# Kernel tuning notes

Hardware: AMD Instinct MI355X
Metric: run time of the kernel (lower is better)

Reference implementation:

```python
import jax, jax.numpy as jnp
import numpy as np

N_NODES = 100000
N_EDGES = 1600000
N_RELS = 19
DIMS = [1, 128, 128, 64]  # in_degree feature -> dims


def setup_inputs() -> dict:
    key = jax.random.key(0)
    ks = jax.random.split(key, 12)
    src = jax.random.randint(ks[0], (N_EDGES,), 0, N_NODES, dtype=jnp.int64)
    dst = jax.random.randint(ks[1], (N_EDGES,), 0, N_NODES, dtype=jnp.int64)
    etypes = jax.random.randint(ks[2], (N_EDGES,), 0, N_RELS, dtype=jnp.int64)
    inp = {"src": src, "dst": dst, "etypes": etypes}
    for i, (din, dout) in enumerate(zip(DIMS[:-1], DIMS[1:])):
        s = 1.0 / np.sqrt(max(din, 1))
        inp[f"W{i}"] = jax.random.normal(ks[3 + 3 * i], (N_RELS, din, dout), jnp.float32) * s
        inp[f"Wloop{i}"] = jax.random.normal(ks[4 + 3 * i], (din, dout), jnp.float32) * s
        inp[f"b{i}"] = jnp.zeros((dout,), jnp.float32)
    inp["num_nodes"] = N_NODES
    return inp


def _rel_graph_conv(h, src, dst, etypes, W, Wloop, b, num_nodes, activation):
    # per-relation transform of every node: [N, R, dout]
    transformed = jnp.einsum('nd,rdo->nro', h, W)
    # gather message per edge by (src node, edge relation): [E, dout]
    msg = transformed[src, etypes]
    # scatter-sum to destination nodes
    agg = jax.ops.segment_sum(msg, dst, num_segments=num_nodes)
    out = agg + h @ Wloop + b
    if activation is not None:
        out = activation(out)
    return out


def reference(src, dst, etypes, W0, Wloop0, b0, W1, Wloop1, b1, W2, Wloop2, b2, num_nodes):
    # h = g.in_degrees().view(-1, 1).float()
    deg = jax.ops.segment_sum(jnp.ones_like(dst, dtype=jnp.float32), dst,
                              num_segments=num_nodes)
    h = deg[:, None]
    h = _rel_graph_conv(h, src, dst, etypes, W0, Wloop0, b0, num_nodes, jax.nn.relu)
    h = _rel_graph_conv(h, src, dst, etypes, W1, Wloop1, b1, num_nodes, jax.nn.relu)
    h = _rel_graph_conv(h, src, dst, etypes, W2, Wloop2, b2, num_nodes, None)
    return h
```

## Files before the change

kernel.cpp:

```cpp
#include <hip/hip_runtime.h>
#include <hip/hip_bf16.h>
#include <stdint.h>

#define N_NODES 100000
#define N_EDGES 1600000
#define N_RELS  19
#define NQ      4
#define QN      25000
#define QTILES  196
#define NBQ     98
#define NSB     (NQ * NBQ)
#define N_BUCK  (NQ * N_RELS)
#define NBIN    391
#define NGR     8
#define NBK8    (N_BUCK * NGR)
#define NBIN8   (NBIN * NGR)
#define NHC     (N_BUCK + NBIN)
#define NHC2    (2 * NHC)
#define MSGQ    460000
#define NCKQ    3700
#define NCK_TOT 14000
#define EPB     2048
#define S1B     782

typedef __attribute__((ext_vector_type(8))) short bf16x8;
typedef __attribute__((ext_vector_type(4))) float f32x4;
typedef __attribute__((ext_vector_type(4))) int   int4v;

__device__ __forceinline__ unsigned short f2bf(float x) {
  union { float f; unsigned u; } v; v.f = x;
  unsigned r = v.u + 0x7FFF + ((v.u >> 16) & 1);
  return (unsigned short)(r >> 16);
}
__device__ __forceinline__ float bf2f(unsigned short b) {
  union { unsigned u; float f; } v; v.u = ((unsigned)b) << 16; return v.f;
}

__global__ void k_prep_w(const float* W1, const float* W2,
                         const float* Wl1, const float* Wl2,
                         unsigned short* Wt1, unsigned short* Wt2,
                         unsigned short* Wtl1, unsigned short* Wtl2) {
  int i = blockIdx.x * 256 + threadIdx.x;
  const int s1 = N_RELS * 128 * 128;
  const int s2 = N_RELS * 64 * 128;
  const int s3 = 128 * 128;
  const int s4 = 64 * 128;
  if (i < s1) {
    int r = i / (128 * 128); int rem = i % (128 * 128);
    int n = rem / 128, k = rem % 128;
    Wt1[i] = f2bf(W1[((size_t)r * 128 + k) * 128 + n]);
  } else if (i < s1 + s2) {
    int j = i - s1;
    int r = j / (64 * 128); int rem = j % (64 * 128);
    int n = rem / 128, k = rem % 128;
    Wt2[j] = f2bf(W2[((size_t)r * 128 + k) * 64 + n]);
  } else if (i < s1 + s2 + s3) {
    int j = i - s1 - s2; int n = j / 128, k = j % 128;
    Wtl1[j] = f2bf(Wl1[k * 128 + n]);
  } else if (i < s1 + s2 + s3 + s4) {
    int j = i - s1 - s2 - s3; int n = j / 128, k = j % 128;
    Wtl2[j] = f2bf(Wl2[k * 64 + n]);
  }
}

__global__ void k_hist(const int* __restrict__ dst, const int* __restrict__ et,
                       int* __restrict__ bcount8, int* __restrict__ bincount8,
                       int* __restrict__ histAll) {
  __shared__ int hK[N_BUCK], hB[NBIN];
  __shared__ int sb[256];
  int t = threadIdx.x, g = blockIdx.x & (NGR - 1);
  for (int i = t; i < N_BUCK; i += 256) hK[i] = 0;
  for (int i = t; i < NBIN; i += 256) hB[i] = 0;
  __syncthreads();
  int e0 = blockIdx.x * EPB;
  for (int r = 0; r < EPB / 256; r++) {
    int e = e0 + r * 256 + t;
    if (e < N_EDGES) {
      int d = dst[e];
      atomicAdd(&hK[(d / QN) * N_RELS + et[e]], 1);
      atomicAdd(&hB[d >> 8], 1);
    }
  }
  __syncthreads();
  int* hout = histAll + (size_t)blockIdx.x * NHC2;
  for (int i = t; i < N_BUCK; i += 256) {
    hout[i] = hK[i];
    if (hK[i]) atomicAdd(&bcount8[i * NGR + g], hK[i]);
  }
  for (int i = t; i < NBIN; i += 256) {
    hout[N_BUCK + i] = hB[i];
    if (hB[i]) atomicAdd(&bincount8[i * NGR + g], hB[i]);
  }
  {
    int v0 = (2 * t < N_BUCK) ? hK[2 * t] : 0;
    int v1 = (2 * t + 1 < N_BUCK) ? hK[2 * t + 1] : 0;
    sb[t] = v0 + v1;
    __syncthreads();
    for (int s = 1; s < 256; s <<= 1) {
      int x = (t >= s) ? sb[t - s] : 0;
      __syncthreads();
      sb[t] += x;
      __syncthreads();
    }
    int base = sb[t] - v0 - v1;
    if (2 * t < N_BUCK) hout[NHC + 2 * t] = base;
    if (2 * t + 1 < N_BUCK) hout[NHC + 2 * t + 1] = base + v0;
    __syncthreads();
  }
  {
    int v0 = (2 * t < NBIN) ? hB[2 * t] : 0;
    int v1 = (2 * t + 1 < NBIN) ? hB[2 * t + 1] : 0;
    sb[t] = v0 + v1;
    __syncthreads();
    for (int s = 1; s < 256; s <<= 1) {
      int x = (t >= s) ? sb[t - s] : 0;
      __syncthreads();
      sb[t] += x;
      __syncthreads();
    }
    int base = sb[t] - v0 - v1;
    if (2 * t < NBIN) hout[NHC + N_BUCK + 2 * t] = base;
    if (2 * t + 1 < NBIN) hout[NHC + N_BUCK + 2 * t + 1] = base + v0;
  }
}

__global__ void k_scan0(const int* __restrict__ bcount8, const int* __restrict__ bincount8,
                        int* boff, int* bcur8, int* cbase, int* qcs, int* selfb,
                        int* binoff8, int* bincur8) {
  __shared__ int shK[NBK8];
  __shared__ int sb76[N_BUCK];
  __shared__ int sbs[N_BUCK];
  __shared__ int sh[512];
  int t = threadIdx.x;
  for (int i = t; i < NBK8; i += 512) shK[i] = bcount8[i];
  __syncthreads();
  if (t < N_BUCK) {
    int s = 0;
    for (int gg = 0; gg < NGR; gg++) s += shK[t * NGR + gg];
    sb76[t] = s;
  }
  __syncthreads();
  if (t == 0) {
    int a = 0, cb = 0;
    for (int q = 0; q < NQ; q++) {
      qcs[q] = cb;
      for (int r = 0; r < N_RELS; r++) {
        int b = q * N_RELS + r;
        boff[b] = a; sbs[b] = a; cbase[b] = cb;
        a += sb76[b]; cb += (sb76[b] + 127) >> 7;
      }
      selfb[q] = cb; cb += QTILES;
    }
    qcs[NQ] = cb;
    boff[N_BUCK] = a;
  }
  __syncthreads();
  for (int i = t; i < NBK8; i += 512) {
    int b = i >> 3, gg = i & (NGR - 1);
    int base = sbs[b];
    for (int k = 0; k < gg; k++) base += shK[b * NGR + k];
    bcur8[i] = base;
  }
  int vals[7];
  int i0 = t * 7;
  int loc = 0;
  for (int k = 0; k < 7; k++) {
    int i = i0 + k;
    int v = (i < NBIN8) ? bincount8[i] : 0;
    vals[k] = v; loc += v;
  }
  sh[t] = loc;
  __syncthreads();
  for (int s = 1; s < 512; s <<= 1) {
    int x = (t >= s) ? sh[t - s] : 0;
    __syncthreads();
    sh[t] += x;
    __syncthreads();
  }
  int run = sh[t] - loc;
  for (int k = 0; k < 7; k++) {
    int i = i0 + k;
    if (i < NBIN8) { binoff8[i] = run; bincur8[i] = run; run += vals[k]; }
  }
  if (t == 511) binoff8[NBIN8] = sh[511];
}

__launch_bounds__(256)
__global__ void k_scat1a(const int* __restrict__ src, const int* __restrict__ dst,
                         const int* __restrict__ et,
                         const int* __restrict__ histAll,
                         int* __restrict__ bcur8,
                         int* __restrict__ srcS, int* __restrict__ posE) {
  __shared__ int sortK[EPB];
  __shared__ int lK[N_BUCK], gKr[N_BUCK];
  int t = threadIdx.x, blk = blockIdx.x, g = blk & (NGR - 1);
  const int* hin = histAll + (size_t)blk * NHC2;
  for (int i = t; i < N_BUCK; i += 256) {
    int h = hin[i], l = hin[NHC + i];
    lK[i] = l;
    gKr[i] = h ? (atomicAdd(&bcur8[i * NGR + g], h) - l) : 0;
  }
  __syncthreads();
  int e0 = blk * EPB;
  int nval = min(EPB, N_EDGES - e0);
  for (int r = 0; r < EPB / 256; r++) {
    int e = e0 + r * 256 + t;
    if (e < N_EDGES) {
      int d = dst[e], rl = et[e], sv = src[e];
      int bk = (d / QN) * N_RELS + rl;
      int lrk = atomicAdd(&lK[bk], 1);
      sortK[lrk] = sv | (bk << 17);
      posE[e] = gKr[bk] + lrk;
    }
  }
  __syncthreads();
  for (int r = 0; r < EPB / 256; r++) {
    int s = r * 256 + t;
    if (s < nval) {
      int v = sortK[s];
      srcS[gKr[v >> 17] + s] = v & 0x1FFFF;
    }
  }
}

__launch_bounds__(256)
__global__ void k_scat1b(const int* __restrict__ src, const int* __restrict__ dst,
                         const int* __restrict__ et,
                         const int* __restrict__ posE,
                         const int* __restrict__ histAll,
                         int* __restrict__ bincur8,
                         int* __restrict__ stgA, int* __restrict__ stgB) {
  __shared__ int sortA[EPB], sortBv[EPB];
  __shared__ int lB[NBIN], gBr[NBIN];
  int t = threadIdx.x, blk = blockIdx.x, g = blk & (NGR - 1);
  const int* hin = histAll + (size_t)blk * NHC2;
  for (int i = t; i < NBIN; i += 256) {
    int h = hin[N_BUCK + i], l = hin[NHC + N_BUCK + i];
    lB[i] = l;
    gBr[i] = h ? (atomicAdd(&bincur8[i * NGR + g], h) - l) : 0;
  }
  __syncthreads();
  int e0 = blk * EPB;
  int nval = min(EPB, N_EDGES - e0);
  for (int r = 0; r < EPB / 256; r++) {
    int e = e0 + r * 256 + t;
    if (e < N_EDGES) {
      int d = dst[e], rl = et[e], sv = src[e];
      int gpos = posE[e];
      int bn = d >> 8;
      int lrb = atomicAdd(&lB[bn], 1);
      sortA[lrb] = gpos | (rl << 21) | ((bn & 63) << 26);
      sortBv[lrb] = sv | ((d & 255) << 17) | ((bn >> 6) << 25);
    }
  }
  __syncthreads();
  for (int r = 0; r < EPB / 256; r++) {
    int s = r * 256 + t;
    if (s < nval) {
      int a = sortA[s], b = sortBv[s];
      int bn = ((a >> 26) & 63) | (((b >> 25) & 7) << 6);
      int adr = gBr[bn] + s;
      stgA[adr] = a & 0x03FFFFFF;
      stgB[adr] = b & 0x01FFFFFF;
    }
  }
}

__global__ void k_cnt(const int* __restrict__ stgB, const int* __restrict__ binoff8,
                      int* __restrict__ ncount) {
  __shared__ int c[256];
  int b = blockIdx.x, t = threadIdx.x;
  c[t] = 0;
  __syncthreads();
  int lo = binoff8[b * NGR], hi = binoff8[b * NGR + NGR];
  for (int s = lo + t; s < hi; s += 256)
    atomicAdd(&c[(stgB[s] >> 17) & 255], 1);
  __syncthreads();
  int n = b * 256 + t;
  if (n < N_NODES) ncount[n] = c[t];
}

__global__ void k_scanA(const int* __restrict__ ncount, int* __restrict__ bsum) {
  __shared__ int sh[256];
  int b = blockIdx.x, t = threadIdx.x;
  int q = b / NBQ, bb = b % NBQ;
  int i = bb * 256 + t;
  int val = (i < QN) ? (ncount[q * QN + i] + 1) : 0;
  sh[t] = val;
  __syncthreads();
  for (int s = 128; s > 0; s >>= 1) {
    if (t < s) sh[t] += sh[t + s];
    __syncthreads();
  }
  if (t == 0) bsum[b] = sh[0];
}

__global__ void k_scanB(const int* bsum, int* bbase, int* nodeoff) {
  __shared__ int sh[NSB];
  int t = threadIdx.x;
  if (t < NSB) sh[t] = bsum[t];
  __syncthreads();
  if (t < NQ) {
    int a = 0;
    for (int i = 0; i < NBQ; i++) {
      int v = sh[t * NBQ + i]; sh[t * NBQ + i] = a; a += v;
    }
    nodeoff[(t + 1) * QN + t] = a;
  }
  __syncthreads();
  if (t < NSB) bbase[t] = sh[t];
}

__global__ void k_scanC(const int* __restrict__ ncount,
                        const int* __restrict__ bbase,
                        const int* __restrict__ boff,
                        int* __restrict__ nodeoff, int* __restrict__ gfwd) {
  __shared__ int sh[256];
  int b = blockIdx.x, t = threadIdx.x;
  int q = b / NBQ, bb = b % NBQ;
  int i = bb * 256 + t;
  int val = (i < QN) ? (ncount[q * QN + i] + 1) : 0;
  sh[t] = val;
  __syncthreads();
  for (int s = 1; s < 256; s <<= 1) {
    int x = (t >= s) ? sh[t - s] : 0;
    __syncthreads();
    sh[t] += x;
    __syncthreads();
  }
  int excl = sh[t] - val + bbase[b];
  if (i < QN) {
    int n = q * QN + i;
    nodeoff[n + q] = excl;
    int qedges = boff[(q + 1) * N_RELS] - boff[q * N_RELS];
    gfwd[(size_t)q * MSGQ + qedges + i] = excl;
  }
}

__global__ void k_scat2(const int* __restrict__ stgA, const int* __restrict__ stgB,
                        const int* __restrict__ binoff8,
                        const int* __restrict__ nodeoff,
                        const int* __restrict__ boff,
                        const int* __restrict__ ncount,
                        int* __restrict__ gfwd, int* __restrict__ Rg) {
  __shared__ int cur[256];
  __shared__ int R[256][N_RELS];
  __shared__ int qe0s[NQ + 1];
  int b = blockIdx.x, t = threadIdx.x;
  if (t <= NQ) qe0s[t] = boff[t * N_RELS];
  int n = b * 256 + t;
  if (n < N_NODES) {
    int q = n / QN;
    cur[t] = nodeoff[n + q] + 1;
  }
#pragma unroll
  for (int r = 0; r < N_RELS; r++) R[t][r] = 0;
  __syncthreads();
  int lo = binoff8[b * NGR], hi = binoff8[b * NGR + NGR];
  for (int s = lo + t; s < hi; s += 256) {
    int a = stgA[s], bb = stgB[s];
    int dlow = (bb >> 17) & 255;
    int slot = atomicAdd(&cur[dlow], 1);
    int pos = a & 0x1FFFFF, rel = (a >> 21) & 31;
    int sv = bb & 0x1FFFF;
    int d = b * 256 + dlow;
    int q = d / QN;
    gfwd[(size_t)q * MSGQ + (pos - qe0s[q])] = slot;
    atomicAdd(&R[dlow][rel], ncount[sv]);
  }
  __syncthreads();
  if (n < N_NODES) {
#pragma unroll
    for (int r = 0; r < N_RELS; r++)
      Rg[(size_t)r * N_NODES + n] = R[t][r];
  }
}

__launch_bounds__(256, 3)
__global__ void k_h1(const int* __restrict__ Rg, const int* __restrict__ ncount,
                     const float* __restrict__ W0, const float* __restrict__ Wl0,
                     const float* __restrict__ b0,
                     unsigned short* __restrict__ h1) {
  __shared__ float W0s[N_RELS * 128];
  __shared__ float wl[128], bb[128];
  __shared__ __align__(16) unsigned short Hs[128 * 128];
  int t = threadIdx.x, blk = blockIdx.x;
  for (int i = t; i < N_RELS * 128; i += 256) W0s[i] = W0[i];
  if (t < 128) { wl[t] = Wl0[t]; bb[t] = b0[t]; }
  __syncthreads();
  int n0 = blk * 128;
  int cnt = min(128, N_NODES - n0);
  int ln = t >> 1;
  int half = (t & 1) * 64;
  if (ln < cnt) {
    int n = n0 + ln;
    float rr[N_RELS];
#pragma unroll
    for (int r = 0; r < N_RELS; r++) rr[r] = (float)Rg[(size_t)r * N_NODES + n];
    float dn = (float)ncount[n];
    for (int c0 = half; c0 < half + 64; c0 += 8) {
      float acc[8];
#pragma unroll
      for (int j = 0; j < 8; j++) acc[j] = dn * wl[c0 + j] + bb[c0 + j];
      for (int r = 0; r < N_RELS; r++) {
#pragma unroll
        for (int j = 0; j < 8; j++)
          acc[j] += rr[r] * W0s[r * 128 + c0 + j];
      }
      unsigned vs[4];
#pragma unroll
      for (int j = 0; j < 4; j++) {
        float x0 = fmaxf(acc[2 * j], 0.f), x1 = fmaxf(acc[2 * j + 1], 0.f);
        vs[j] = (unsigned)f2bf(x0) | ((unsigned)f2bf(x1) << 16);
      }
      int4v o = {(int)vs[0], (int)vs[1], (int)vs[2], (int)vs[3]};
      *(int4v*)&Hs[ln * 128 + c0] = o;
    }
  }
  __syncthreads();
  int tot = cnt * 16;
  for (int task = t; task < tot; task += 256)
    *(int4v*)&h1[(size_t)n0 * 128 + task * 8] = *(const int4v*)&Hs[task * 8];
}

__global__ void k_fill(const int* boff, const int* cbase,
                       const int* selfb, int* cA, int* cB) {
  int b = blockIdx.x;
  if (b < N_BUCK) {
    int cnt = boff[b + 1] - boff[b], e0 = boff[b], w0 = cbase[b];
    int rel = b % N_RELS;
    int nch = (cnt + 127) >> 7;
    for (int i = threadIdx.x; i < nch; i += blockDim.x) {
      cA[w0 + i] = (e0 + i * 128) | (rel << 21);
      cB[w0 + i] = min(128, cnt - i * 128);
    }
  } else {
    int q = b - N_BUCK;
    int w0 = selfb[q];
    for (int i = threadIdx.x; i < QTILES; i += blockDim.x) {
      cA[w0 + i] = (i * 128) | (19 << 21);
      cB[w0 + i] = min(128, QN - i * 128);
    }
  }
}

template <int NOUT>
__launch_bounds__(256, NOUT == 64 ? 5 : 4)
__global__ void k_gemm_msg(const unsigned short* __restrict__ hprev,
                           const unsigned short* __restrict__ Wt,
                           const unsigned short* __restrict__ Wtl,
                           const int* __restrict__ qcs, int q,
                           const int* __restrict__ cA,
                           const int* __restrict__ cB,
                           const int* __restrict__ srcS,
                           const int* __restrict__ boff,
                           const int* __restrict__ gfwd,
                           unsigned short* __restrict__ msg) {
  const int LDK = 136;
  const int CLD = NOUT + 8;
  const int SH = (NOUT * LDK > 128 * CLD) ? NOUT * LDK : 128 * CLD;
  __shared__ __align__(16) unsigned short Bs[SH];

  int cs = qcs[q], ce = qcs[q + 1];
  int w = blockIdx.x;
  if (w >= ce - cs) return;
  w += cs;
  int pa = cA[w];
  int e0 = pa & 0x1FFFFF, rel = pa >> 21;
  int cnt = cB[w];
  bool self = (rel == 19);
  const unsigned short* wsrc = self ? Wtl : (Wt + (size_t)rel * NOUT * 128);
  int qe0 = boff[q * N_RELS];
  int qedges = boff[(q + 1) * N_RELS] - qe0;
  int ppos0 = self ? (qedges + e0) : (e0 - qe0);
  int tid = threadIdx.x;
  const int lane = tid & 63, wid = tid >> 6;

  int rowg[2]; bool valv[2];
#pragma unroll
  for (int fi = 0; fi < 2; fi++) {
    int m = wid * 32 + fi * 16 + (lane & 15);
    bool v = m < cnt;
    valv[fi] = v;
    int row = 0;
    if (v) row = self ? (q * QN + e0 + m) : srcS[e0 + m];
    rowg[fi] = row;
  }
  bf16x8 a[2][4];
#pragma unroll
  for (int fi = 0; fi < 2; fi++) {
    const unsigned short* rp = hprev + (size_t)rowg[fi] * 128 + (lane >> 4) * 8;
#pragma unroll
    for (int kk = 0; kk < 4; kk++)
      a[fi][kk] = *(const bf16x8*)&rp[kk * 32];
  }
#pragma unroll
  for (int fi = 0; fi < 2; fi++)
    if (!valv[fi]) {
#pragma unroll
      for (int kk = 0; kk < 4; kk++)
        a[fi][kk] = (bf16x8){0, 0, 0, 0, 0, 0, 0, 0};
    }

  for (int task = tid; task < NOUT * 16; task += 256) {
    int n = task >> 4, c = task & 15;
    *(int4v*)&Bs[n * LDK + c * 8] = *(const int4v*)&wsrc[n * 128 + c * 8];
  }
  __syncthreads();

  const int FJ = NOUT / 16;
  f32x4 acc[2][FJ];
#pragma unroll
  for (int i = 0; i < 2; i++)
#pragma unroll
    for (int j = 0; j < FJ; j++) acc[i][j] = (f32x4){0.f, 0.f, 0.f, 0.f};

#pragma unroll
  for (int kk = 0; kk < 4; kk++) {
    int kof = kk * 32 + (lane >> 4) * 8;
    bf16x8 b[FJ];
#pragma unroll
    for (int fj = 0; fj < FJ; fj++)
      b[fj] = *(const bf16x8*)&Bs[(fj * 16 + (lane & 15)) * LDK + kof];
#pragma unroll
    for (int fi = 0; fi < 2; fi++)
#pragma unroll
      for (int fj = 0; fj < FJ; fj++)
        acc[fi][fj] = __builtin_amdgcn_mfma_f32_16x16x32_bf16(a[fi][kk], b[fj], acc[fi][fj], 0, 0, 0);
  }

  __syncthreads();
#pragma unroll
  for (int fi = 0; fi < 2; fi++)
#pragma unroll
    for (int fj = 0; fj < FJ; fj++)
#pragma unroll
      for (int j = 0; j < 4; j++) {
        int mrow = wid * 32 + fi * 16 + (lane >> 4) * 4 + j;
        int col = fj * 16 + (lane & 15);
        Bs[mrow * CLD + col] = f2bf(acc[fi][fj][j]);
      }
  __syncthreads();
  const int CW = NOUT / 8;
  for (int task = tid; task < cnt * CW; task += 256) {
    int row = task / CW, c = task % CW;
    int slot = gfwd[ppos0 + row];
    *(int4v*)&msg[(size_t)slot * NOUT + c * 8] =
        *(const int4v*)&Bs[row * CLD + c * 8];
  }
}

template <int NOUT>
__global__ void k_reduce(const unsigned short* __restrict__ msg,
                         const int* __restrict__ nodeoff, int q,
                         const float* __restrict__ bias, int do_relu,
                         unsigned short* __restrict__ outh,
                         float* __restrict__ outf) {
  int t = threadIdx.x;
  int rn = blockIdx.x * 8 + (t >> 5);
  if (rn >= QN) return;
  int n = q * QN + rn;
  int l = t & 31;
  int lo = nodeoff[n + q], hi = nodeoff[n + q + 1];
  if (NOUT == 128) {
    float a0 = 0.f, a1 = 0.f, a2 = 0.f, a3 = 0.f;
    for (int i = lo; i < hi; i++) {
      uint2 v = *(const uint2*)&msg[(size_t)i * 128 + l * 4];
      a0 += bf2f((unsigned short)(v.x & 0xffff));
      a1 += bf2f((unsigned short)(v.x >> 16));
      a2 += bf2f((unsigned short)(v.y & 0xffff));
      a3 += bf2f((unsigned short)(v.y >> 16));
    }
    a0 += bias[l * 4];     a1 += bias[l * 4 + 1];
    a2 += bias[l * 4 + 2]; a3 += bias[l * 4 + 3];
    if (do_relu) {
      a0 = fmaxf(a0, 0.f); a1 = fmaxf(a1, 0.f);
      a2 = fmaxf(a2, 0.f); a3 = fmaxf(a3, 0.f);
    }
    uint2 o;
    o.x = (unsigned)f2bf(a0) | ((unsigned)f2bf(a1) << 16);
    o.y = (unsigned)f2bf(a2) | ((unsigned)f2bf(a3) << 16);
    *(uint2*)&outh[(size_t)n * 128 + l * 4] = o;
  } else {
    float a0 = 0.f, a1 = 0.f;
    for (int i = lo; i < hi; i++) {
      unsigned v = *(const unsigned*)&msg[(size_t)i * 64 + l * 2];
      a0 += bf2f((unsigned short)(v & 0xffff));
      a1 += bf2f((unsigned short)(v >> 16));
    }
    a0 += bias[l * 2];
    a1 += bias[l * 2 + 1];
    if (do_relu) { a0 = fmaxf(a0, 0.f); a1 = fmaxf(a1, 0.f); }
    outf[(size_t)n * 64 + l * 2]     = a0;
    outf[(size_t)n * 64 + l * 2 + 1] = a1;
  }
}

extern "C" void kernel_launch(void* const* d_in, const int* in_sizes, int n_in,
                              void* d_out, int out_size, void* d_ws, size_t ws_size,
                              hipStream_t stream) {
  const int* src = (const int*)d_in[0];
  const int* dst = (const int*)d_in[1];
  const int* et  = (const int*)d_in[2];
  const float* W0  = (const float*)d_in[3];
  const float* Wl0 = (const float*)d_in[4];
  const float* b0  = (const float*)d_in[5];
  const float* W1  = (const float*)d_in[6];
  const float* Wl1 = (const float*)d_in[7];
  const float* b1  = (const float*)d_in[8];
  const float* W2  = (const float*)d_in[9];
  const float* Wl2 = (const float*)d_in[10];
  const float* b2  = (const float*)d_in[11];

  char* ws = (char*)d_ws;
  size_t off = 0;
  auto alloc = [&](size_t bytes) {
    void* p = ws + off;
    off = (off + bytes + 255) & ~(size_t)255;
    return p;
  };
  unsigned short* msg = (unsigned short*)alloc((size_t)MSGQ * 128 * 2);
  unsigned short* h1 = (unsigned short*)alloc((size_t)N_NODES * 128 * 2);
  unsigned short* h2 = (unsigned short*)alloc((size_t)N_NODES * 128 * 2);
  int* srcS = (int*)alloc((size_t)N_EDGES * 4);
  int* stgA = (int*)alloc((size_t)N_EDGES * 4);
  int* stgB = (int*)alloc((size_t)N_EDGES * 4);
  int* posE = (int*)alloc((size_t)N_EDGES * 4);
  int* gfwd = (int*)alloc((size_t)NQ * MSGQ * 4);
  int* Rg   = (int*)alloc((size_t)N_RELS * N_NODES * 4);
  int* ncount  = (int*)alloc((size_t)N_NODES * 4);
  int* nodeoff = (int*)alloc((size_t)(N_NODES + NQ + 4) * 4);
  int* histAll = (int*)alloc((size_t)S1B * NHC2 * 4);
  unsigned short* Wt1  = (unsigned short*)alloc((size_t)N_RELS * 128 * 128 * 2);
  unsigned short* Wt2  = (unsigned short*)alloc((size_t)N_RELS * 64 * 128 * 2);
  unsigned short* Wtl1 = (unsigned short*)alloc((size_t)128 * 128 * 2);
  unsigned short* Wtl2 = (unsigned short*)alloc((size_t)64 * 128 * 2);
  int* acc0 = (int*)alloc((size_t)(NBK8 + NBIN8) * 4);
  int* bcount8   = acc0;
  int* bincount8 = acc0 + NBK8;
  int* ints = (int*)alloc(4096);
  int* boff   = ints;
  int* cbase  = ints + 80;
  int* qcs    = ints + 160;
  int* selfb  = ints + 168;
  int* bcur8  = (int*)alloc((size_t)NBK8 * 4);
  int* binoff8 = (int*)alloc((size_t)(NBIN8 + 1) * 4);
  int* bincur8 = (int*)alloc((size_t)NBIN8 * 4);
  int* bsum  = (int*)alloc((size_t)NSB * 4);
  int* bbase = (int*)alloc((size_t)NSB * 4);
  int* cA = (int*)alloc((size_t)NCK_TOT * 4);
  int* cB = (int*)alloc((size_t)NCK_TOT * 4);

  hipMemsetAsync(acc0, 0, (size_t)(NBK8 + NBIN8) * 4, stream);

  k_prep_w<<<1920, 256, 0, stream>>>(W1, W2, Wl1, Wl2, Wt1, Wt2, Wtl1, Wtl2);
  k_hist<<<S1B, 256, 0, stream>>>(dst, et, bcount8, bincount8, histAll);
  k_scan0<<<1, 512, 0, stream>>>(bcount8, bincount8, boff, bcur8, cbase, qcs,
                                 selfb, binoff8, bincur8);
  k_scat1a<<<S1B, 256, 0, stream>>>(src, dst, et, histAll, bcur8, srcS, posE);
  k_scat1b<<<S1B, 256, 0, stream>>>(src, dst, et, posE, histAll, bincur8,
                                    stgA, stgB);
  k_cnt<<<NBIN, 256, 0, stream>>>(stgB, binoff8, ncount);
  k_scanA<<<NSB, 256, 0, stream>>>(ncount, bsum);
  k_scanB<<<1, 512, 0, stream>>>(bsum, bbase, nodeoff);
  k_scanC<<<NSB, 256, 0, stream>>>(ncount, bbase, boff, nodeoff, gfwd);
  k_scat2<<<NBIN, 256, 0, stream>>>(stgA, stgB, binoff8, nodeoff, boff,
                                    ncount, gfwd, Rg);
  k_fill<<<N_BUCK + NQ, 256, 0, stream>>>(boff, cbase, selfb, cA, cB);
  k_h1<<<(N_NODES + 127) / 128, 256, 0, stream>>>(Rg, ncount, W0, Wl0, b0, h1);

  for (int q = 0; q < NQ; q++) {
    k_gemm_msg<128><<<NCKQ, 256, 0, stream>>>(h1, Wt1, Wtl1, qcs, q, cA, cB,
                                              srcS, boff,
                                              gfwd + (size_t)q * MSGQ, msg);
    k_reduce<128><<<QN / 8, 256, 0, stream>>>(msg, nodeoff, q, b1, 1,
                                              h2, nullptr);
  }
  for (int q = 0; q < NQ; q++) {
    k_gemm_msg<64><<<NCKQ, 256, 0, stream>>>(h2, Wt2, Wtl2, qcs, q, cA, cB,
                                             srcS, boff,
                                             gfwd + (size_t)q * MSGQ, msg);
    k_reduce<64><<<QN / 8, 256, 0, stream>>>(msg, nodeoff, q, b2, 0,
                                             nullptr, (float*)d_out);
  }
}
```

Measured before the change: 658.4 us.

## Batch two node quarters per layer-2 GEMM/reduce launch and widen scat2 blocks

Layer-2 message GEMM and reduce kernels now handle two node quarters per launch, using separate message buffer halves. This halves the number of launches and gives each launch more blocks, so there are fewer tail and idle phases. The 64-wide messages for two quarters still fit in the buffer that held one 128-wide quarter. k_scat2 also runs 512 threads per block to spread the per-bin edge loop over more threads, at the cost of more shared-memory atomic contention.

Result: faster. 628.1 us (-4.6%).

```diff
diff --git a/kernel.cpp b/kernel.cpp
--- a/kernel.cpp
+++ b/kernel.cpp
@@ -337,6 +337,7 @@
   }
 }
 
+__launch_bounds__(512)
 __global__ void k_scat2(const int* __restrict__ stgA, const int* __restrict__ stgB,
                         const int* __restrict__ binoff8,
                         const int* __restrict__ nodeoff,
@@ -348,16 +349,18 @@
   __shared__ int qe0s[NQ + 1];
   int b = blockIdx.x, t = threadIdx.x;
   if (t <= NQ) qe0s[t] = boff[t * N_RELS];
-  int n = b * 256 + t;
-  if (n < N_NODES) {
-    int q = n / QN;
-    cur[t] = nodeoff[n + q] + 1;
-  }
-#pragma unroll
-  for (int r = 0; r < N_RELS; r++) R[t][r] = 0;
+  if (t < 256) {
+    int n = b * 256 + t;
+    if (n < N_NODES) {
+      int q = n / QN;
+      cur[t] = nodeoff[n + q] + 1;
+    }
+#pragma unroll
+    for (int r = 0; r < N_RELS; r++) R[t][r] = 0;
+  }
   __syncthreads();
   int lo = binoff8[b * NGR], hi = binoff8[b * NGR + NGR];
-  for (int s = lo + t; s < hi; s += 256) {
+  for (int s = lo + t; s < hi; s += 512) {
     int a = stgA[s], bb = stgB[s];
     int dlow = (bb >> 17) & 255;
     int slot = atomicAdd(&cur[dlow], 1);
@@ -369,10 +372,13 @@
     atomicAdd(&R[dlow][rel], ncount[sv]);
   }
   __syncthreads();
-  if (n < N_NODES) {
-#pragma unroll
-    for (int r = 0; r < N_RELS; r++)
-      Rg[(size_t)r * N_NODES + n] = R[t][r];
+  if (t < 256) {
+    int n = b * 256 + t;
+    if (n < N_NODES) {
+#pragma unroll
+      for (int r = 0; r < N_RELS; r++)
+        Rg[(size_t)r * N_NODES + n] = R[t][r];
+    }
   }
 }
 
@@ -449,7 +455,7 @@
 __global__ void k_gemm_msg(const unsigned short* __restrict__ hprev,
                            const unsigned short* __restrict__ Wt,
                            const unsigned short* __restrict__ Wtl,
-                           const int* __restrict__ qcs, int q,
+                           const int* __restrict__ qcs, int q0, int nqp,
                            const int* __restrict__ cA,
                            const int* __restrict__ cB,
                            const int* __restrict__ srcS,
@@ -461,18 +467,22 @@
   const int SH = (NOUT * LDK > 128 * CLD) ? NOUT * LDK : 128 * CLD;
   __shared__ __align__(16) unsigned short Bs[SH];
 
-  int cs = qcs[q], ce = qcs[q + 1];
+  int cs = qcs[q0], ce = qcs[q0 + nqp];
   int w = blockIdx.x;
   if (w >= ce - cs) return;
   w += cs;
+  int qq = q0;
+  if (nqp == 2 && w >= qcs[q0 + 1]) qq = q0 + 1;
   int pa = cA[w];
   int e0 = pa & 0x1FFFFF, rel = pa >> 21;
   int cnt = cB[w];
   bool self = (rel == 19);
   const unsigned short* wsrc = self ? Wtl : (Wt + (size_t)rel * NOUT * 128);
-  int qe0 = boff[q * N_RELS];
-  int qedges = boff[(q + 1) * N_RELS] - qe0;
+  int qe0 = boff[qq * N_RELS];
+  int qedges = boff[(qq + 1) * N_RELS] - qe0;
   int ppos0 = self ? (qedges + e0) : (e0 - qe0);
+  const int* gf = gfwd + (size_t)qq * MSGQ;
+  unsigned short* msgq = msg + (size_t)(qq - q0) * MSGQ * NOUT;
   int tid = threadIdx.x;
   const int lane = tid & 63, wid = tid >> 6;
 
@@ -483,7 +493,7 @@
     bool v = m < cnt;
     valv[fi] = v;
     int row = 0;
-    if (v) row = self ? (q * QN + e0 + m) : srcS[e0 + m];
+    if (v) row = self ? (qq * QN + e0 + m) : srcS[e0 + m];
     rowg[fi] = row;
   }
   bf16x8 a[2][4];
@@ -544,28 +554,31 @@
   const int CW = NOUT / 8;
   for (int task = tid; task < cnt * CW; task += 256) {
     int row = task / CW, c = task % CW;
-    int slot = gfwd[ppos0 + row];
-    *(int4v*)&msg[(size_t)slot * NOUT + c * 8] =
+    int slot = gf[ppos0 + row];
+    *(int4v*)&msgq[(size_t)slot * NOUT + c * 8] =
         *(const int4v*)&Bs[row * CLD + c * 8];
   }
 }
 
 template <int NOUT>
 __global__ void k_reduce(const unsigned short* __restrict__ msg,
-                         const int* __restrict__ nodeoff, int q,
+                         const int* __restrict__ nodeoff, int q0,
                          const float* __restrict__ bias, int do_relu,
                          unsigned short* __restrict__ outh,
                          float* __restrict__ outf) {
   int t = threadIdx.x;
-  int rn = blockIdx.x * 8 + (t >> 5);
+  const int bpq = QN / 8;
+  int qq = q0 + blockIdx.x / bpq;
+  int rn = (blockIdx.x % bpq) * 8 + (t >> 5);
   if (rn >= QN) return;
-  int n = q * QN + rn;
+  int n = qq * QN + rn;
   int l = t & 31;
-  int lo = nodeoff[n + q], hi = nodeoff[n + q + 1];
+  int lo = nodeoff[n + qq], hi = nodeoff[n + qq + 1];
+  const unsigned short* m = msg + (size_t)(qq - q0) * MSGQ * NOUT;
   if (NOUT == 128) {
     float a0 = 0.f, a1 = 0.f, a2 = 0.f, a3 = 0.f;
     for (int i = lo; i < hi; i++) {
-      uint2 v = *(const uint2*)&msg[(size_t)i * 128 + l * 4];
+      uint2 v = *(const uint2*)&m[(size_t)i * 128 + l * 4];
       a0 += bf2f((unsigned short)(v.x & 0xffff));
       a1 += bf2f((unsigned short)(v.x >> 16));
       a2 += bf2f((unsigned short)(v.y & 0xffff));
@@ -584,7 +597,7 @@
   } else {
     float a0 = 0.f, a1 = 0.f;
     for (int i = lo; i < hi; i++) {
-      unsigned v = *(const unsigned*)&msg[(size_t)i * 64 + l * 2];
+      unsigned v = *(const unsigned*)&m[(size_t)i * 64 + l * 2];
       a0 += bf2f((unsigned short)(v & 0xffff));
       a1 += bf2f((unsigned short)(v >> 16));
     }
@@ -664,23 +677,22 @@
   k_scanA<<<NSB, 256, 0, stream>>>(ncount, bsum);
   k_scanB<<<1, 512, 0, stream>>>(bsum, bbase, nodeoff);
   k_scanC<<<NSB, 256, 0, stream>>>(ncount, bbase, boff, nodeoff, gfwd);
-  k_scat2<<<NBIN, 256, 0, stream>>>(stgA, stgB, binoff8, nodeoff, boff,
+  k_scat2<<<NBIN, 512, 0, stream>>>(stgA, stgB, binoff8, nodeoff, boff,
                                     ncount, gfwd, Rg);
   k_fill<<<N_BUCK + NQ, 256, 0, stream>>>(boff, cbase, selfb, cA, cB);
   k_h1<<<(N_NODES + 127) / 128, 256, 0, stream>>>(Rg, ncount, W0, Wl0, b0, h1);
 
   for (int q = 0; q < NQ; q++) {
-    k_gemm_msg<128><<<NCKQ, 256, 0, stream>>>(h1, Wt1, Wtl1, qcs, q, cA, cB,
-                                              srcS, boff,
-                                              gfwd + (size_t)q * MSGQ, msg);
+    k_gemm_msg<128><<<NCKQ, 256, 0, stream>>>(h1, Wt1, Wtl1, qcs, q, 1, cA, cB,
+                                              srcS, boff, gfwd, msg);
     k_reduce<128><<<QN / 8, 256, 0, stream>>>(msg, nodeoff, q, b1, 1,
                                               h2, nullptr);
   }
-  for (int q = 0; q < NQ; q++) {
-    k_gemm_msg<64><<<NCKQ, 256, 0, stream>>>(h2, Wt2, Wtl2, qcs, q, cA, cB,
-                                             srcS, boff,
-                                             gfwd + (size_t)q * MSGQ, msg);
-    k_reduce<64><<<QN / 8, 256, 0, stream>>>(msg, nodeoff, q, b2, 0,
-                                             nullptr, (float*)d_out);
-  }
-}
+  for (int qp = 0; qp < 2; qp++) {
+    int q0 = 2 * qp;
+    k_gemm_msg<64><<<2 * NCKQ, 256, 0, stream>>>(h2, Wt2, Wtl2, qcs, q0, 2,
+                                                 cA, cB, srcS, boff, gfwd, msg);
+    k_reduce<64><<<2 * (QN / 8), 256, 0, stream>>>(msg, nodeoff, q0, b2, 0,
+                                                   nullptr, (float*)d_out);
+  }
+}
```
